# Performance work log

Measured on AMD Instinct MI355X. Metric: run time of the kernel, lower is better.

## Reference

```python
import jax, jax.numpy as jnp
import numpy as np

N = 100000
H = 512
NUM_HEADS = 8
G = 512  # number of graphs (segments)


def seg_softmax(s, batch, num_segments):
    # numerically stable segment softmax (PyG-style, +1e-16 in denom)
    m = jax.ops.segment_max(s, batch, num_segments=num_segments)
    e = jnp.exp(s - m[batch])
    d = jax.ops.segment_sum(e, batch, num_segments=num_segments)
    return e / (d[batch] + 1e-16)


def setup_inputs() -> dict:
    key = jax.random.key(0)
    ks = jax.random.split(key, 12)
    s = 0.02
    x = jax.random.normal(ks[0], (N, H), dtype=jnp.float32)
    batch = jnp.sort(jax.random.randint(ks[1], (N,), 0, G)).astype(jnp.int64)
    # GlobalAttention.gate_nn: Linear(H, H//2) -> ReLU -> Linear(H//2, 1)
    ga_g_w1 = jax.random.normal(ks[2], (H, H // 2), dtype=jnp.float32) * s
    ga_g_b1 = jnp.zeros((H // 2,), dtype=jnp.float32)
    ga_g_w2 = jax.random.normal(ks[3], (H // 2, 1), dtype=jnp.float32) * s
    ga_g_b2 = jnp.zeros((1,), dtype=jnp.float32)
    # GlobalAttention.nn: Linear(H, H) -> ReLU
    ga_n_w = jax.random.normal(ks[4], (H, H), dtype=jnp.float32) * s
    ga_n_b = jnp.zeros((H,), dtype=jnp.float32)
    # outer gate_nn: Linear(H, H) -> ReLU -> (Dropout: identity in eval) -> Linear(H, NUM_HEADS)
    g_w1 = jax.random.normal(ks[5], (H, H), dtype=jnp.float32) * s
    g_b1 = jnp.zeros((H,), dtype=jnp.float32)
    g_w2 = jax.random.normal(ks[6], (H, NUM_HEADS), dtype=jnp.float32) * s
    g_b2 = jnp.zeros((NUM_HEADS,), dtype=jnp.float32)
    return dict(x=x, batch=batch,
                ga_g_w1=ga_g_w1, ga_g_b1=ga_g_b1, ga_g_w2=ga_g_w2, ga_g_b2=ga_g_b2,
                ga_n_w=ga_n_w, ga_n_b=ga_n_b,
                g_w1=g_w1, g_b1=g_b1, g_w2=g_w2, g_b2=g_b2)


def reference(x, batch, ga_g_w1, ga_g_b1, ga_g_w2, ga_g_b2, ga_n_w, ga_n_b,
              g_w1, g_b1, g_w2, g_b2):
    # --- GlobalAttention pooling ---
    h = jax.nn.relu(x @ ga_g_w1 + ga_g_b1)          # (N, H//2)
    gate = (h @ ga_g_w2 + ga_g_b2)[:, 0]            # (N,)
    gate = seg_softmax(gate, batch, G)              # segment softmax per graph
    xt = jax.nn.relu(x @ ga_n_w + ga_n_b)           # (N, H)
    graph_embedding = jax.ops.segment_sum(gate[:, None] * xt, batch,
                                          num_segments=G)  # (G, H)
    # --- interpretable attention weights ---
    g = jax.nn.relu(x @ g_w1 + g_b1)                # (N, H); dropout = identity (eval)
    scores = (g @ g_w2 + g_b2).mean(axis=-1)        # (N,) mean over heads
    attention = seg_softmax(scores, batch, G)       # (N,)
    return graph_embedding, attention
```

## Files before the change

kernel.cpp:

```cpp
#include <hip/hip_runtime.h>

#define NN 100000
#define HH 512
#define GG 512
#define NPACK 1280
#define NSTRIP 40
#define SB 32768
#define XTROWS (NN + 128)

typedef unsigned short u16;
typedef __bf16 bf16x8 __attribute__((ext_vector_type(8)));
typedef unsigned short u16x8 __attribute__((ext_vector_type(8)));
typedef float f32x4 __attribute__((ext_vector_type(4)));
typedef __attribute__((address_space(1))) void gvoid_t;
typedef __attribute__((address_space(3))) void lvoid_t;

__device__ __forceinline__ u16 f2bf(float f) {
    unsigned u = __float_as_uint(f);
    unsigned r = u + 0x7FFFu + ((u >> 16) & 1u);
    return (u16)(r >> 16);
}
__device__ __forceinline__ float bf2f(u16 b) {
    return __uint_as_float(((unsigned)b) << 16);
}

__global__ void k_prep(const float* __restrict__ gw1, const float* __restrict__ gb1,
                       const float* __restrict__ gw2v,
                       const float* __restrict__ nw, const float* __restrict__ nb,
                       const float* __restrict__ aw1, const float* __restrict__ ab1,
                       const float* __restrict__ aw2, const int* __restrict__ batch,
                       u16* __restrict__ WT, float2* __restrict__ bwv,
                       float* __restrict__ out_emb, int* __restrict__ starts) {
    int idx = blockIdx.x * blockDim.x + threadIdx.x;
    int stride = gridDim.x * blockDim.x;
    for (int i = idx; i < NPACK * 512; i += stride) {
        int n = i >> 9, k = i & 511;
        float v;
        if (n < 256)      v = gw1[k * 256 + n];
        else if (n < 768) v = nw[k * 512 + (n - 256)];
        else              v = aw1[k * 512 + (n - 768)];
        int s = n >> 5, nl = n & 31;
        int ck = k >> 3, k3 = k & 7;
        size_t byte = (size_t)s * SB + nl * 1024 + ((size_t)(ck ^ (nl & 15)) << 4) + k3 * 2;
        *(u16*)((char*)WT + byte) = f2bf(v);
    }
    for (int n = idx; n < NPACK; n += stride) {
        float bi, wv;
        if (n < 256)      { bi = gb1[n];       wv = gw2v[n]; }
        else if (n < 768) { bi = nb[n - 256];  wv = 0.f; }
        else {
            bi = ab1[n - 768];
            float s = 0.f;
            for (int h = 0; h < 8; ++h) s += aw2[(n - 768) * 8 + h];
            wv = s * 0.125f;
        }
        bwv[n] = make_float2(bi, wv);
    }
    for (int i = idx; i < GG * HH; i += stride) out_emb[i] = 0.f;
    for (int g = idx; g <= GG; g += stride) {
        if (g == GG) { starts[GG] = NN; continue; }
        int lo = 0, hi = NN;
        while (lo < hi) { int mid = (lo + hi) >> 1; if (batch[mid] < g) lo = mid + 1; else hi = mid; }
        starts[g] = lo;
    }
}

__global__ __launch_bounds__(256, 2)
void k_gemm(const float* __restrict__ X, const u16* __restrict__ B,
            const float2* __restrict__ bwv,
            const float* __restrict__ gb2, const float* __restrict__ ab2,
            u16* __restrict__ xt, float* __restrict__ gs, float* __restrict__ as_) {
    __shared__ __align__(16) char ldsB[2 * SB];

    const int tid = threadIdx.x;
    const int lane = tid & 63;
    const int w = tid >> 6;
    const int m0 = blockIdx.x * 128;
    const int l16 = lane & 15, kq = lane >> 4;

#define STAGE(s, bsel) do {                                                          \
    const char* _src = (const char*)B + (size_t)(s) * SB + tid * 16;                 \
    char* _dst = ldsB + (bsel) * SB + tid * 16;                                      \
    _Pragma("unroll")                                                                \
    for (int _t = 0; _t < 8; ++_t)                                                   \
        __builtin_amdgcn_global_load_lds((gvoid_t*)(_src + _t * 4096),               \
                                         (lvoid_t*)(_dst + _t * 4096), 16, 0, 0);    \
} while (0)

    STAGE(0, 0);

    float b2 = gb2[0];
    float bb = 0.f;
#pragma unroll
    for (int h = 0; h < 8; ++h) bb += ab2[h];
    bb *= 0.125f;

    bf16x8 a_reg[2][16];
#pragma unroll
    for (int i = 0; i < 2; ++i) {
        int row = m0 + w * 32 + i * 16 + l16;
        if (row >= NN) row = NN - 1;
        const float* xp = X + (size_t)row * 512 + kq * 8;
#pragma unroll
        for (int kt = 0; kt < 16; ++kt) {
            float4 f0 = *(const float4*)(xp + kt * 32);
            float4 f1 = *(const float4*)(xp + kt * 32 + 4);
            u16x8 u;
            u[0] = f2bf(f0.x); u[1] = f2bf(f0.y); u[2] = f2bf(f0.z); u[3] = f2bf(f0.w);
            u[4] = f2bf(f1.x); u[5] = f2bf(f1.y); u[6] = f2bf(f1.z); u[7] = f2bf(f1.w);
            a_reg[i][kt] = __builtin_bit_cast(bf16x8, u);
        }
    }

    float sg[2][4], sa[2][4];
#pragma unroll
    for (int i = 0; i < 2; ++i)
#pragma unroll
        for (int r = 0; r < 4; ++r) { sg[i][r] = 0.f; sa[i][r] = 0.f; }

    for (int nt = 0; nt < NSTRIP; ++nt) {
        const int cur = nt & 1;

        float2 bw0 = bwv[nt * 32 + l16];
        float2 bw1 = bwv[nt * 32 + 16 + l16];

        if (nt + 1 < NSTRIP) STAGE(nt + 1, cur ^ 1);

        if (nt == NSTRIP - 1)         asm volatile("s_waitcnt vmcnt(0)" ::: "memory");
        else if (nt >= 9 && nt <= 24) asm volatile("s_waitcnt vmcnt(18)" ::: "memory");
        else                          asm volatile("s_waitcnt vmcnt(10)" ::: "memory");
        __builtin_amdgcn_s_barrier();
        __builtin_amdgcn_sched_barrier(0);

        f32x4 acc[2][2];
#pragma unroll
        for (int i = 0; i < 2; ++i) { acc[i][0] = {0.f,0.f,0.f,0.f}; acc[i][1] = {0.f,0.f,0.f,0.f}; }

        const char* bbase = ldsB + cur * SB + l16 * 1024;
#pragma unroll
        for (int kt = 0; kt < 16; ++kt) {
            int off = ((kt * 4 + kq) ^ l16) << 4;
            bf16x8 b0 = *(const bf16x8*)(bbase + off);
            bf16x8 b1 = *(const bf16x8*)(bbase + 16384 + off);
#pragma unroll
            for (int i = 0; i < 2; ++i) {
                acc[i][0] = __builtin_amdgcn_mfma_f32_16x16x32_bf16(a_reg[i][kt], b0, acc[i][0], 0, 0, 0);
                acc[i][1] = __builtin_amdgcn_mfma_f32_16x16x32_bf16(a_reg[i][kt], b1, acc[i][1], 0, 0, 0);
            }
        }
        __builtin_amdgcn_s_barrier();

        if (nt >= 8 && nt < 24) {
            const int sx = nt - 8;
#pragma unroll
            for (int i = 0; i < 2; ++i)
#pragma unroll
                for (int r = 0; r < 4; ++r) {
                    int rg = m0 + w * 32 + i * 16 + kq * 4 + r;
                    ushort2 st;
                    st.x = f2bf(fmaxf(acc[i][0][r] + bw0.x, 0.f));
                    st.y = f2bf(fmaxf(acc[i][1][r] + bw1.x, 0.f));
                    *(ushort2*)(xt + (size_t)rg * 512 + sx * 32 + l16 * 2) = st;
                }
        } else if (nt < 8) {
#pragma unroll
            for (int i = 0; i < 2; ++i)
#pragma unroll
                for (int r = 0; r < 4; ++r)
                    sg[i][r] += fmaxf(acc[i][0][r] + bw0.x, 0.f) * bw0.y
                              + fmaxf(acc[i][1][r] + bw1.x, 0.f) * bw1.y;
        } else {
#pragma unroll
            for (int i = 0; i < 2; ++i)
#pragma unroll
                for (int r = 0; r < 4; ++r)
                    sa[i][r] += fmaxf(acc[i][0][r] + bw0.x, 0.f) * bw0.y
                              + fmaxf(acc[i][1][r] + bw1.x, 0.f) * bw1.y;
        }
    }
#undef STAGE

#pragma unroll
    for (int i = 0; i < 2; ++i)
#pragma unroll
        for (int r = 0; r < 4; ++r) {
            float pg = sg[i][r], pa = sa[i][r];
            pg += __shfl_xor(pg, 1); pg += __shfl_xor(pg, 2);
            pg += __shfl_xor(pg, 4); pg += __shfl_xor(pg, 8);
            pa += __shfl_xor(pa, 1); pa += __shfl_xor(pa, 2);
            pa += __shfl_xor(pa, 4); pa += __shfl_xor(pa, 8);
            int rg = m0 + w * 32 + i * 16 + kq * 4 + r;
            if (l16 == 0 && rg < NN) {
                gs[rg] = pg + b2;
                as_[rg] = pa + bb;
            }
        }
}

__global__ void k_seg(const float* __restrict__ gs, const float* __restrict__ as_,
                      const int* __restrict__ starts,
                      float* __restrict__ mg, float* __restrict__ dg,
                      float* __restrict__ ma, float* __restrict__ da) {
    int g = blockIdx.x;
    int s0 = starts[g], s1 = starts[g + 1];
    int tid = threadIdx.x, lane = tid & 63, w = tid >> 6;
    __shared__ float red[8];
    float lmg = -3.0e38f, lma = -3.0e38f;
    for (int i = s0 + tid; i < s1; i += 256) {
        lmg = fmaxf(lmg, gs[i]); lma = fmaxf(lma, as_[i]);
    }
    for (int o = 32; o; o >>= 1) {
        lmg = fmaxf(lmg, __shfl_xor(lmg, o));
        lma = fmaxf(lma, __shfl_xor(lma, o));
    }
    if (lane == 0) { red[w] = lmg; red[4 + w] = lma; }
    __syncthreads();
    float Mg = fmaxf(fmaxf(red[0], red[1]), fmaxf(red[2], red[3]));
    float Ma = fmaxf(fmaxf(red[4], red[5]), fmaxf(red[6], red[7]));
    __syncthreads();
    float sgv = 0.f, sav = 0.f;
    for (int i = s0 + tid; i < s1; i += 256) {
        sgv += expf(gs[i] - Mg); sav += expf(as_[i] - Ma);
    }
    for (int o = 32; o; o >>= 1) { sgv += __shfl_xor(sgv, o); sav += __shfl_xor(sav, o); }
    if (lane == 0) { red[w] = sgv; red[4 + w] = sav; }
    __syncthreads();
    if (tid == 0) {
        mg[g] = Mg; ma[g] = Ma;
        dg[g] = red[0] + red[1] + red[2] + red[3];
        da[g] = red[4] + red[5] + red[6] + red[7];
    }
}

__global__ void k_final(const float* __restrict__ gs, const float* __restrict__ as_,
                        const int* __restrict__ batch,
                        const float* __restrict__ mg, const float* __restrict__ dg,
                        const float* __restrict__ ma, const float* __restrict__ da,
                        float* __restrict__ gate, float* __restrict__ attn) {
    int stride = gridDim.x * blockDim.x;
    for (int i = blockIdx.x * blockDim.x + threadIdx.x; i < NN; i += stride) {
        int b = batch[i];
        gate[i] = expf(gs[i] - mg[b]) / (dg[b] + 1e-16f);
        attn[i] = expf(as_[i] - ma[b]) / (da[b] + 1e-16f);
    }
}

__global__ void k_emb(const u16* __restrict__ xt, const float* __restrict__ gate,
                      const int* __restrict__ starts, float* __restrict__ out) {
    int g = blockIdx.y;
    int part = blockIdx.x;
    int s0 = starts[g], s1 = starts[g + 1];
    int len = s1 - s0;
    int p0 = s0 + (len * part) / 4, p1 = s0 + (len * (part + 1)) / 4;
    int c2 = threadIdx.x;
    int col0 = (c2 >> 4) * 32 + (c2 & 15);
    float a0 = 0.f, a1 = 0.f;
    for (int n = p0; n < p1; ++n) {
        float gn = gate[n];
        ushort2 u = reinterpret_cast<const ushort2*>(xt + (size_t)n * 512)[c2];
        a0 += gn * bf2f(u.x);
        a1 += gn * bf2f(u.y);
    }
    atomicAdd(&out[g * 512 + col0], a0);
    atomicAdd(&out[g * 512 + col0 + 16], a1);
}

extern "C" void kernel_launch(void* const* d_in, const int* in_sizes, int n_in,
                              void* d_out, int out_size, void* d_ws, size_t ws_size,
                              hipStream_t stream) {
    const float* x       = (const float*)d_in[0];
    const int*   batch   = (const int*)d_in[1];
    const float* ga_g_w1 = (const float*)d_in[2];
    const float* ga_g_b1 = (const float*)d_in[3];
    const float* ga_g_w2 = (const float*)d_in[4];
    const float* ga_g_b2 = (const float*)d_in[5];
    const float* ga_n_w  = (const float*)d_in[6];
    const float* ga_n_b  = (const float*)d_in[7];
    const float* g_w1    = (const float*)d_in[8];
    const float* g_b1    = (const float*)d_in[9];
    const float* g_w2    = (const float*)d_in[10];
    const float* g_b2    = (const float*)d_in[11];

    float* out_emb = (float*)d_out;
    float* out_att = out_emb + GG * HH;

    char* p = (char*)d_ws;
    size_t off = 0;
    auto alloc = [&](size_t bytes) -> char* {
        char* q = p + off;
        off += (bytes + 255) & ~(size_t)255;
        return q;
    };
    u16*    xt    = (u16*)   alloc((size_t)XTROWS * HH * 2);
    u16*    WT    = (u16*)   alloc((size_t)NPACK * 512 * 2);
    float2* bwv   = (float2*)alloc(NPACK * 8);
    float*  gs    = (float*) alloc((size_t)NN * 4);
    float*  as_   = (float*) alloc((size_t)NN * 4);
    float*  gate  = (float*) alloc((size_t)NN * 4);
    float*  mg    = (float*) alloc(GG * 4);
    float*  dg    = (float*) alloc(GG * 4);
    float*  ma    = (float*) alloc(GG * 4);
    float*  da    = (float*) alloc(GG * 4);
    int*    starts= (int*)   alloc((GG + 1) * 4);

    k_prep<<<2560, 256, 0, stream>>>(ga_g_w1, ga_g_b1, ga_g_w2, ga_n_w, ga_n_b,
                                     g_w1, g_b1, g_w2, batch, WT, bwv, out_emb, starts);
    k_gemm<<<782, 256, 0, stream>>>(x, WT, bwv, ga_g_b2, g_b2, xt, gs, as_);
    k_seg<<<GG, 256, 0, stream>>>(gs, as_, starts, mg, dg, ma, da);
    k_final<<<400, 256, 0, stream>>>(gs, as_, batch, mg, dg, ma, da, gate, out_att);
    k_emb<<<dim3(4, GG), 256, 0, stream>>>(xt, gate, starts, out_emb);
}
```

Baseline: 469.7 us.

## Halve GEMM N-strip width to shrink LDS and registers for three-block occupancy

The fused GEMM now processes 16-column weight strips instead of 32, so LDS staging drops to 2x16KB and the accumulators halve, which permits launch_bounds occupancy of 3 blocks per CU. The xt output is built by stashing packed bf16 values from even strips and writing them together with odd strips, which keeps the 32-column store pattern. Gate-score reductions are finished mid-loop, and bias loads are prefetched one strip ahead. The loop also sets s_setprio around the MFMA section. The trade-off is twice as many barriers and strip iterations, with less MFMA work per barrier.

```diff
diff --git a/kernel.cpp b/kernel.cpp
--- a/kernel.cpp
+++ b/kernel.cpp
@@ -4,11 +4,12 @@
 #define HH 512
 #define GG 512
 #define NPACK 1280
-#define NSTRIP 40
-#define SB 32768
+#define NSTRIP 80
+#define SB 16384
 #define XTROWS (NN + 128)
 
 typedef unsigned short u16;
+typedef unsigned int u32;
 typedef __bf16 bf16x8 __attribute__((ext_vector_type(8)));
 typedef unsigned short u16x8 __attribute__((ext_vector_type(8)));
 typedef float f32x4 __attribute__((ext_vector_type(4)));
@@ -39,16 +40,16 @@
         if (n < 256)      v = gw1[k * 256 + n];
         else if (n < 768) v = nw[k * 512 + (n - 256)];
         else              v = aw1[k * 512 + (n - 768)];
-        int s = n >> 5, nl = n & 31;
+        int s = n >> 4, nl = n & 15;
         int ck = k >> 3, k3 = k & 7;
-        size_t byte = (size_t)s * SB + nl * 1024 + ((size_t)(ck ^ (nl & 15)) << 4) + k3 * 2;
+        size_t byte = (size_t)s * SB + nl * 1024 + ((size_t)(ck ^ nl) << 4) + k3 * 2;
         *(u16*)((char*)WT + byte) = f2bf(v);
     }
-    for (int n = idx; n < NPACK; n += stride) {
-        float bi, wv;
+    for (int n = idx; n < NPACK + 16; n += stride) {
+        float bi = 0.f, wv = 0.f;
         if (n < 256)      { bi = gb1[n];       wv = gw2v[n]; }
         else if (n < 768) { bi = nb[n - 256];  wv = 0.f; }
-        else {
+        else if (n < NPACK) {
             bi = ab1[n - 768];
             float s = 0.f;
             for (int h = 0; h < 8; ++h) s += aw2[(n - 768) * 8 + h];
@@ -65,7 +66,7 @@
     }
 }
 
-__global__ __launch_bounds__(256, 2)
+__global__ __launch_bounds__(256, 3)
 void k_gemm(const float* __restrict__ X, const u16* __restrict__ B,
             const float2* __restrict__ bwv,
             const float* __restrict__ gb2, const float* __restrict__ ab2,
@@ -82,7 +83,7 @@
     const char* _src = (const char*)B + (size_t)(s) * SB + tid * 16;                 \
     char* _dst = ldsB + (bsel) * SB + tid * 16;                                      \
     _Pragma("unroll")                                                                \
-    for (int _t = 0; _t < 8; ++_t)                                                   \
+    for (int _t = 0; _t < 4; ++_t)                                                   \
         __builtin_amdgcn_global_load_lds((gvoid_t*)(_src + _t * 4096),               \
                                          (lvoid_t*)(_dst + _t * 4096), 16, 0, 0);    \
 } while (0)
@@ -112,71 +113,97 @@
         }
     }
 
-    float sg[2][4], sa[2][4];
+    float2 bw = bwv[l16];
+
+    float s_[2][4];
 #pragma unroll
     for (int i = 0; i < 2; ++i)
 #pragma unroll
-        for (int r = 0; r < 4; ++r) { sg[i][r] = 0.f; sa[i][r] = 0.f; }
+        for (int r = 0; r < 4; ++r) s_[i][r] = 0.f;
+    u32 stash[4];
 
     for (int nt = 0; nt < NSTRIP; ++nt) {
         const int cur = nt & 1;
-
-        float2 bw0 = bwv[nt * 32 + l16];
-        float2 bw1 = bwv[nt * 32 + 16 + l16];
-
         if (nt + 1 < NSTRIP) STAGE(nt + 1, cur ^ 1);
 
-        if (nt == NSTRIP - 1)         asm volatile("s_waitcnt vmcnt(0)" ::: "memory");
-        else if (nt >= 9 && nt <= 24) asm volatile("s_waitcnt vmcnt(18)" ::: "memory");
-        else                          asm volatile("s_waitcnt vmcnt(10)" ::: "memory");
+        if (nt == NSTRIP - 1)
+            asm volatile("s_waitcnt vmcnt(0)" ::: "memory");
+        else if (nt >= 18 && nt <= 48 && !(nt & 1))
+            asm volatile("s_waitcnt vmcnt(13)" ::: "memory");
+        else
+            asm volatile("s_waitcnt vmcnt(5)" ::: "memory");
         __builtin_amdgcn_s_barrier();
         __builtin_amdgcn_sched_barrier(0);
 
-        f32x4 acc[2][2];
-#pragma unroll
-        for (int i = 0; i < 2; ++i) { acc[i][0] = {0.f,0.f,0.f,0.f}; acc[i][1] = {0.f,0.f,0.f,0.f}; }
+        f32x4 acc[2];
+        acc[0] = {0.f, 0.f, 0.f, 0.f};
+        acc[1] = {0.f, 0.f, 0.f, 0.f};
 
         const char* bbase = ldsB + cur * SB + l16 * 1024;
+        __builtin_amdgcn_s_setprio(1);
 #pragma unroll
         for (int kt = 0; kt < 16; ++kt) {
             int off = ((kt * 4 + kq) ^ l16) << 4;
             bf16x8 b0 = *(const bf16x8*)(bbase + off);
-            bf16x8 b1 = *(const bf16x8*)(bbase + 16384 + off);
-#pragma unroll
-            for (int i = 0; i < 2; ++i) {
-                acc[i][0] = __builtin_amdgcn_mfma_f32_16x16x32_bf16(a_reg[i][kt], b0, acc[i][0], 0, 0, 0);
-                acc[i][1] = __builtin_amdgcn_mfma_f32_16x16x32_bf16(a_reg[i][kt], b1, acc[i][1], 0, 0, 0);
+            acc[0] = __builtin_amdgcn_mfma_f32_16x16x32_bf16(a_reg[0][kt], b0, acc[0], 0, 0, 0);
+            acc[1] = __builtin_amdgcn_mfma_f32_16x16x32_bf16(a_reg[1][kt], b0, acc[1], 0, 0, 0);
+        }
+        __builtin_amdgcn_s_setprio(0);
+        __builtin_amdgcn_s_barrier();
+
+        float2 bw_next = bwv[(nt + 1) * 16 + l16];
+
+        if (nt < 16) {
+#pragma unroll
+            for (int i = 0; i < 2; ++i)
+#pragma unroll
+                for (int r = 0; r < 4; ++r)
+                    s_[i][r] += fmaxf(acc[i][r] + bw.x, 0.f) * bw.y;
+            if (nt == 15) {
+#pragma unroll
+                for (int i = 0; i < 2; ++i)
+#pragma unroll
+                    for (int r = 0; r < 4; ++r) {
+                        float pg = s_[i][r];
+                        pg += __shfl_xor(pg, 1); pg += __shfl_xor(pg, 2);
+                        pg += __shfl_xor(pg, 4); pg += __shfl_xor(pg, 8);
+                        int rg = m0 + w * 32 + i * 16 + kq * 4 + r;
+                        if (l16 == 0 && rg < NN) gs[rg] = pg + b2;
+                        s_[i][r] = 0.f;
+                    }
             }
-        }
-        __builtin_amdgcn_s_barrier();
-
-        if (nt >= 8 && nt < 24) {
-            const int sx = nt - 8;
+        } else if (nt < 48) {
+            const int sx = nt - 16;
+            if (!(sx & 1)) {
+#pragma unroll
+                for (int i = 0; i < 2; ++i)
+#pragma unroll
+                    for (int rp = 0; rp < 2; ++rp) {
+                        u32 lo = f2bf(fmaxf(acc[i][rp * 2]     + bw.x, 0.f));
+                        u32 hi = f2bf(fmaxf(acc[i][rp * 2 + 1] + bw.x, 0.f));
+                        stash[i * 2 + rp] = lo | (hi << 16);
+                    }
+            } else {
+                const int s2 = sx >> 1;
+#pragma unroll
+                for (int i = 0; i < 2; ++i)
+#pragma unroll
+                    for (int r = 0; r < 4; ++r) {
+                        int rg = m0 + w * 32 + i * 16 + kq * 4 + r;
+                        ushort2 st;
+                        st.x = (u16)(stash[i * 2 + (r >> 1)] >> ((r & 1) * 16));
+                        st.y = f2bf(fmaxf(acc[i][r] + bw.x, 0.f));
+                        *(ushort2*)(xt + (size_t)rg * 512 + s2 * 32 + l16 * 2) = st;
+                    }
+            }
+        } else {
 #pragma unroll
             for (int i = 0; i < 2; ++i)
 #pragma unroll
-                for (int r = 0; r < 4; ++r) {
-                    int rg = m0 + w * 32 + i * 16 + kq * 4 + r;
-                    ushort2 st;
-                    st.x = f2bf(fmaxf(acc[i][0][r] + bw0.x, 0.f));
-                    st.y = f2bf(fmaxf(acc[i][1][r] + bw1.x, 0.f));
-                    *(ushort2*)(xt + (size_t)rg * 512 + sx * 32 + l16 * 2) = st;
-                }
-        } else if (nt < 8) {
-#pragma unroll
-            for (int i = 0; i < 2; ++i)
-#pragma unroll
                 for (int r = 0; r < 4; ++r)
-                    sg[i][r] += fmaxf(acc[i][0][r] + bw0.x, 0.f) * bw0.y
-                              + fmaxf(acc[i][1][r] + bw1.x, 0.f) * bw1.y;
-        } else {
-#pragma unroll
-            for (int i = 0; i < 2; ++i)
-#pragma unroll
-                for (int r = 0; r < 4; ++r)
-                    sa[i][r] += fmaxf(acc[i][0][r] + bw0.x, 0.f) * bw0.y
-                              + fmaxf(acc[i][1][r] + bw1.x, 0.f) * bw1.y;
-        }
+                    s_[i][r] += fmaxf(acc[i][r] + bw.x, 0.f) * bw.y;
+        }
+        bw = bw_next;
     }
 #undef STAGE
 
@@ -184,16 +211,11 @@
     for (int i = 0; i < 2; ++i)
 #pragma unroll
         for (int r = 0; r < 4; ++r) {
-            float pg = sg[i][r], pa = sa[i][r];
-            pg += __shfl_xor(pg, 1); pg += __shfl_xor(pg, 2);
-            pg += __shfl_xor(pg, 4); pg += __shfl_xor(pg, 8);
+            float pa = s_[i][r];
             pa += __shfl_xor(pa, 1); pa += __shfl_xor(pa, 2);
             pa += __shfl_xor(pa, 4); pa += __shfl_xor(pa, 8);
             int rg = m0 + w * 32 + i * 16 + kq * 4 + r;
-            if (l16 == 0 && rg < NN) {
-                gs[rg] = pg + b2;
-                as_[rg] = pa + bb;
-            }
+            if (l16 == 0 && rg < NN) as_[rg] = pa + bb;
         }
 }
 
@@ -293,7 +315,7 @@
     };
     u16*    xt    = (u16*)   alloc((size_t)XTROWS * HH * 2);
     u16*    WT    = (u16*)   alloc((size_t)NPACK * 512 * 2);
-    float2* bwv   = (float2*)alloc(NPACK * 8);
+    float2* bwv   = (float2*)alloc((NPACK + 16) * 8);
     float*  gs    = (float*) alloc((size_t)NN * 4);
     float*  as_   = (float*) alloc((size_t)NN * 4);
     float*  gate  = (float*) alloc((size_t)NN * 4);
```

After: 823.5 us. 1.75x slower.
